# Performance work log

Hardware: AMD Instinct MI355X
Metric: run time of the kernel (lower is better)

Reference implementation:

```python
import jax, jax.numpy as jnp
import numpy as np

N, E = 50000, 600000
DIMS = [128, 256, 256, 256, 256, 64]  # in, h1..h4, out


def setup_inputs() -> dict:
    key = jax.random.key(0)
    ks = jax.random.split(key, 12)
    inp = {
        "x": jax.random.normal(ks[0], (N, DIMS[0]), dtype=jnp.float32),
        "edge_index": jax.random.randint(ks[1], (2, E), 0, N, dtype=jnp.int64 if jax.config.jax_enable_x64 else jnp.int32),
    }
    for i in range(5):
        fi, fo = DIMS[i], DIMS[i + 1]
        s = 1.0 / np.sqrt(fi)  # glorot-ish uniform, matching GCNConv default scale
        inp[f"W{i+1}"] = jax.random.uniform(ks[2 + 2 * i], (fi, fo), jnp.float32, -s, s)
        inp[f"b{i+1}"] = jnp.zeros((fo,), jnp.float32)
    return inp


def _gcn_norm(edge_index, n):
    # Add self-loops and compute symmetric normalization D^-1/2 (A+I) D^-1/2.
    loop = jnp.arange(n, dtype=edge_index.dtype)
    src = jnp.concatenate([edge_index[0], loop])  # [E+N]
    dst = jnp.concatenate([edge_index[1], loop])
    deg = jax.ops.segment_sum(jnp.ones_like(dst, dtype=jnp.float32), dst, num_segments=n)
    dinv = jnp.where(deg > 0, jax.lax.rsqrt(deg), 0.0)
    norm = dinv[src] * dinv[dst]  # [E+N]
    return src, dst, norm


def _gcn_layer(x, src, dst, norm, W, b, n):
    h = x @ W                       # [N, Fo] linear transform first (fewer msg bytes)
    msg = h[src] * norm[:, None]    # gather + edge-weight scale
    out = jax.ops.segment_sum(msg, dst, num_segments=n)  # scatter-add aggregate
    return out + b


def reference(x, edge_index, W1, b1, W2, b2, W3, b3, W4, b4, W5, b5):
    n = x.shape[0]
    src, dst, norm = _gcn_norm(edge_index, n)
    params = [(W1, b1), (W2, b2), (W3, b3), (W4, b4), (W5, b5)]
    h = x
    for i, (W, b) in enumerate(params):
        h = _gcn_layer(h, src, dst, norm, W, b, n)
        if i < 4:
            h = jax.nn.relu(h)  # dropout is identity in eval mode
    return h
```

## Files before the change

kernel.cpp:

```cpp
#include <hip/hip_runtime.h>
#include <stdint.h>


typedef _Float16 v8h __attribute__((ext_vector_type(8)));
typedef _Float16 v4h __attribute__((ext_vector_type(4)));
typedef float v4f __attribute__((ext_vector_type(4)));

__global__ void count_edges(const int* __restrict__ dst, int E, int* __restrict__ counts) {
    int i = blockIdx.x * blockDim.x + threadIdx.x;
    if (i < E) atomicAdd(&counts[dst[i]], 1);
}

__global__ void block_sums(const int* __restrict__ counts, int n, int* __restrict__ partial) {
    __shared__ int red[256];
    int t = threadIdx.x;
    int i = blockIdx.x * 256 + t;
    red[t] = (i < n) ? counts[i] : 0;
    __syncthreads();
    #pragma unroll
    for (int off = 128; off > 0; off >>= 1) {
        if (t < off) red[t] += red[t + off];
        __syncthreads();
    }
    if (t == 0) partial[blockIdx.x] = red[0];
}

__global__ void scan_partials(int* __restrict__ partial, int nb, int* __restrict__ row_ptr, int n) {
    __shared__ int s[256];
    int t = threadIdx.x;
    int v = (t < nb) ? partial[t] : 0;
    s[t] = v;
    __syncthreads();
    #pragma unroll
    for (int off = 1; off < 256; off <<= 1) {
        int u = (t >= off) ? s[t - off] : 0;
        __syncthreads();
        s[t] += u;
        __syncthreads();
    }
    if (t < nb) partial[t] = s[t] - v;
    if (t == 0) row_ptr[n] = s[255];
}

__global__ void scan_final(const int* __restrict__ counts, int n, const int* __restrict__ partial,
                           int* __restrict__ row_ptr, float* __restrict__ dinv,
                           int* __restrict__ fill) {
    __shared__ int s[256];
    int t = threadIdx.x;
    int i = blockIdx.x * 256 + t;
    int c = (i < n) ? counts[i] : 0;
    s[t] = c;
    __syncthreads();
    #pragma unroll
    for (int off = 1; off < 256; off <<= 1) {
        int u = (t >= off) ? s[t - off] : 0;
        __syncthreads();
        s[t] += u;
        __syncthreads();
    }
    if (i < n) {
        row_ptr[i] = partial[blockIdx.x] + s[t] - c;
        dinv[i] = rsqrtf((float)(c + 1));
        fill[i] = 0;
    }
}

__global__ void build_csr(const int* __restrict__ src, const int* __restrict__ dst, int E,
                          const int* __restrict__ row_ptr, int* __restrict__ fill,
                          int* __restrict__ ssrc) {
    int i = blockIdx.x * blockDim.x + threadIdx.x;
    if (i < E) {
        int d = dst[i];
        int pos = row_ptr[d] + atomicAdd(&fill[d], 1);
        ssrc[pos] = src[i];
    }
}

__global__ void split_w(const float* __restrict__ W, _Float16* __restrict__ Wh,
                        _Float16* __restrict__ Wl, int FI, int FO) {
    int i = blockIdx.x * 256 + threadIdx.x;
    if (i < FI * FO) {
        int c = i / FI, k = i - c * FI;
        float v = W[(size_t)k * FO + c];
        _Float16 h = (_Float16)v;
        Wh[i] = h;
        Wl[i] = (_Float16)(v - (float)h);
    }
}

template <int F, bool HILO_IN, bool SPLIT_OUT>
__global__ void agg_kernel(const float* __restrict__ inF,
                           const _Float16* __restrict__ inH, const _Float16* __restrict__ inL,
                           const int* __restrict__ row_ptr, const int* __restrict__ ssrc,
                           const float* __restrict__ dinv, const float* __restrict__ bias,
                           _Float16* __restrict__ outH, _Float16* __restrict__ outL,
                           float* __restrict__ outF, int n) {
    constexpr int VE = F / 64;
    int wid = (blockIdx.x * blockDim.x + threadIdx.x) >> 6;
    if (wid >= n) return;
    int lane = threadIdx.x & 63;
    const float dd = dinv[wid];
    float acc[VE];

    auto load_row = [&](int row, float* v) {
        if constexpr (HILO_IN) {
            v4h h = *(const v4h*)&inH[(size_t)row * F + lane * 4];
            v4h l = *(const v4h*)&inL[(size_t)row * F + lane * 4];
            #pragma unroll
            for (int j = 0; j < 4; ++j) v[j] = (float)h[j] + (float)l[j];
        } else if constexpr (VE == 4) {
            float4 t = *(const float4*)&inF[(size_t)row * F + lane * 4];
            v[0] = t.x; v[1] = t.y; v[2] = t.z; v[3] = t.w;
        } else if constexpr (VE == 2) {
            float2 t = *(const float2*)&inF[(size_t)row * F + lane * 2];
            v[0] = t.x; v[1] = t.y;
        } else {
            v[0] = inF[(size_t)row * F + lane];
        }
    };

    {
        float v[VE];
        load_row(wid, v);
        #pragma unroll
        for (int j = 0; j < VE; ++j) acc[j] = dd * v[j];
    }
    int e = row_ptr[wid];
    const int end = row_ptr[wid + 1];
    for (; e + 1 < end; e += 2) {
        int s0 = ssrc[e], s1 = ssrc[e + 1];
        float w0 = dinv[s0], w1 = dinv[s1];
        float v0[VE], v1[VE];
        load_row(s0, v0);
        load_row(s1, v1);
        #pragma unroll
        for (int j = 0; j < VE; ++j) acc[j] += w0 * v0[j];
        #pragma unroll
        for (int j = 0; j < VE; ++j) acc[j] += w1 * v1[j];
    }
    if (e < end) {
        int s = ssrc[e];
        float w = dinv[s];
        float v[VE];
        load_row(s, v);
        #pragma unroll
        for (int j = 0; j < VE; ++j) acc[j] += w * v[j];
    }

    if constexpr (SPLIT_OUT) {
        _Float16 hs[VE], ls[VE];
        #pragma unroll
        for (int j = 0; j < VE; ++j) {
            float s = dd * acc[j];
            _Float16 h = (_Float16)s;
            hs[j] = h;
            ls[j] = (_Float16)(s - (float)h);
        }
        size_t o = (size_t)wid * F + lane * VE;
        #pragma unroll
        for (int j = 0; j < VE; ++j) { outH[o + j] = hs[j]; outL[o + j] = ls[j]; }
    } else {
        #pragma unroll
        for (int j = 0; j < VE; ++j) {
            float s = dd * acc[j];
            if (bias) s += bias[lane * VE + j];
            outF[(size_t)wid * F + lane * VE + j] = s;
        }
    }
}

__device__ __forceinline__ void gl_lds16(const _Float16* g, _Float16* l) {
    __builtin_amdgcn_global_load_lds(
        (const __attribute__((address_space(1))) uint32_t*)g,
        (__attribute__((address_space(3))) uint32_t*)l, 16, 0, 0);
}

template <int FI, int FO, int MODE>
__global__ __launch_bounds__(256) void gemm_mfma(
    const _Float16* __restrict__ Ah, const _Float16* __restrict__ Al,
    const _Float16* __restrict__ Wth, const _Float16* __restrict__ Wtl,
    const float* __restrict__ bias,
    _Float16* __restrict__ Oh, _Float16* __restrict__ Ol,
    float* __restrict__ Of, int n) {
    constexpr int BK = 32;
    constexpr int NSTEP = FI / BK;
    __shared__ _Float16 lds[12288];
    const int m0 = blockIdx.x * 128;
    const int n0 = blockIdx.y * 64;
    const int t = threadIdx.x;
    const int w = t >> 6;
    const int lane = t & 63;

    const int G0 = w * 128 + lane;
    const int G1 = G0 + 64;
    const int arow0 = (G0 >> 6) * 16 + (G0 & 15), akc0 = ((G0 >> 4) & 3) * 8;
    const int arow1 = (G1 >> 6) * 16 + (G1 & 15), akc1 = ((G1 >> 4) & 3) * 8;
    const _Float16* sAh0 = Ah + (size_t)(m0 + arow0) * FI + akc0;
    const _Float16* sAh1 = Ah + (size_t)(m0 + arow1) * FI + akc1;
    const _Float16* sAl0 = Al + (size_t)(m0 + arow0) * FI + akc0;
    const _Float16* sAl1 = Al + (size_t)(m0 + arow1) * FI + akc1;
    const int bcol = w * 16 + (lane & 15), bkc = (lane >> 4) * 8;
    const _Float16* sBh = Wth + (size_t)(n0 + bcol) * FI + bkc;
    const _Float16* sBl = Wtl + (size_t)(n0 + bcol) * FI + bkc;

    _Float16* dAh0 = &lds[w * 1024];
    _Float16* dAh1 = &lds[w * 1024 + 512];
    _Float16* dAl0 = &lds[4096 + w * 1024];
    _Float16* dAl1 = &lds[4096 + w * 1024 + 512];
    _Float16* dBh = &lds[8192 + w * 512];
    _Float16* dBl = &lds[10240 + w * 512];

    const int wm = w >> 1, wn = w & 1;
    v4f acc[4][2];
    #pragma unroll
    for (int i = 0; i < 4; ++i)
        #pragma unroll
        for (int j = 0; j < 2; ++j) acc[i][j] = (v4f){0.f, 0.f, 0.f, 0.f};

    for (int s = 0; s < NSTEP; ++s) {
        const int ko = s * BK;
        gl_lds16(sAh0 + ko, dAh0);
        gl_lds16(sAh1 + ko, dAh1);
        gl_lds16(sAl0 + ko, dAl0);
        gl_lds16(sAl1 + ko, dAl1);
        gl_lds16(sBh + ko, dBh);
        gl_lds16(sBl + ko, dBl);
        __syncthreads();
        v8h ah[4], al[4], bh[2], bl[2];
        #pragma unroll
        for (int i = 0; i < 4; ++i) {
            ah[i] = *(const v8h*)&lds[(wm * 4 + i) * 512 + lane * 8];
            al[i] = *(const v8h*)&lds[4096 + (wm * 4 + i) * 512 + lane * 8];
        }
        #pragma unroll
        for (int j = 0; j < 2; ++j) {
            bh[j] = *(const v8h*)&lds[8192 + (wn * 2 + j) * 512 + lane * 8];
            bl[j] = *(const v8h*)&lds[10240 + (wn * 2 + j) * 512 + lane * 8];
        }
        #pragma unroll
        for (int i = 0; i < 4; ++i)
            #pragma unroll
            for (int j = 0; j < 2; ++j) {
                acc[i][j] = __builtin_amdgcn_mfma_f32_16x16x32_f16(ah[i], bh[j], acc[i][j], 0, 0, 0);
                acc[i][j] = __builtin_amdgcn_mfma_f32_16x16x32_f16(ah[i], bl[j], acc[i][j], 0, 0, 0);
                acc[i][j] = __builtin_amdgcn_mfma_f32_16x16x32_f16(al[i], bh[j], acc[i][j], 0, 0, 0);
            }
        __syncthreads();
    }

    const int rl = (lane >> 4) * 4;
    const int cl = lane & 15;
    #pragma unroll
    for (int j = 0; j < 2; ++j) {
        const int gcol = n0 + wn * 32 + j * 16 + cl;
        float bv = (MODE == 0) ? bias[gcol] : 0.f;
        #pragma unroll
        for (int i = 0; i < 4; ++i) {
            const int grow = m0 + wm * 64 + i * 16 + rl;
            #pragma unroll
            for (int r = 0; r < 4; ++r) {
                if (grow + r < n) {
                    float v = acc[i][j][r];
                    if (MODE == 0) {
                        v = fmaxf(v + bv, 0.f);
                        _Float16 h = (_Float16)v;
                        Oh[(size_t)(grow + r) * FO + gcol] = h;
                        Ol[(size_t)(grow + r) * FO + gcol] = (_Float16)(v - (float)h);
                    } else {
                        Of[(size_t)(grow + r) * FO + gcol] = v;
                    }
                }
            }
        }
    }
}

extern "C" void kernel_launch(void* const* d_in, const int* in_sizes, int n_in,
                              void* d_out, int out_size, void* d_ws, size_t ws_size,
                              hipStream_t stream) {
    const float* x = (const float*)d_in[0];
    const int* ei = (const int*)d_in[1];
    const int E = in_sizes[1] / 2;
    const int n = in_sizes[0] / 128;
    const int* esrc = ei;
    const int* edst = ei + E;
    const float* W[5] = {(const float*)d_in[2], (const float*)d_in[4], (const float*)d_in[6],
                         (const float*)d_in[8], (const float*)d_in[10]};
    const float* b[5] = {(const float*)d_in[3], (const float*)d_in[5], (const float*)d_in[7],
                         (const float*)d_in[9], (const float*)d_in[11]};
    float* out = (float*)d_out;
    const int NPAD = ((n + 127) / 128) * 128;

    char* ws = (char*)d_ws;
    auto carve = [&](size_t bytes) {
        char* p = ws;
        ws += (bytes + 255) & ~(size_t)255;
        return p;
    };
    int* counts = (int*)carve((size_t)n * 4);
    int* row_ptr = (int*)carve((size_t)(n + 1) * 4);
    int* fill = (int*)carve((size_t)n * 4);
    float* dinv = (float*)carve((size_t)n * 4);
    int* partial = (int*)carve(1024);
    int* ssrc = (int*)carve((size_t)E * 4);
    const int FIs[5] = {128, 256, 256, 256, 256};
    const int FOs[5] = {256, 256, 256, 256, 64};
    _Float16 *Wh[5], *Wl[5];
    for (int l = 0; l < 5; ++l) {
        Wh[l] = (_Float16*)carve((size_t)FIs[l] * FOs[l] * 2);
        Wl[l] = (_Float16*)carve((size_t)FIs[l] * FOs[l] * 2);
    }
    _Float16* Ah = (_Float16*)carve((size_t)NPAD * 256 * 2);
    _Float16* Al = (_Float16*)carve((size_t)NPAD * 256 * 2);
    _Float16* Bh = (_Float16*)carve((size_t)NPAD * 256 * 2);
    _Float16* Bl = (_Float16*)carve((size_t)NPAD * 256 * 2);
    float* scratch = (float*)Ah;

    hipMemsetAsync(counts, 0, (size_t)n * 4, stream);
    count_edges<<<(E + 255) / 256, 256, 0, stream>>>(edst, E, counts);
    const int nsb = (n + 255) / 256;
    block_sums<<<nsb, 256, 0, stream>>>(counts, n, partial);
    scan_partials<<<1, 256, 0, stream>>>(partial, nsb, row_ptr, n);
    scan_final<<<nsb, 256, 0, stream>>>(counts, n, partial, row_ptr, dinv, fill);
    build_csr<<<(E + 255) / 256, 256, 0, stream>>>(esrc, edst, E, row_ptr, fill, ssrc);
    for (int l = 0; l < 5; ++l) {
        int sz = FIs[l] * FOs[l];
        split_w<<<(sz + 255) / 256, 256, 0, stream>>>(W[l], Wh[l], Wl[l], FIs[l], FOs[l]);
    }

    const int aggBlocks = (n + 3) / 4;
    const dim3 g4(NPAD / 128, 4), g1(NPAD / 128, 1);

    agg_kernel<128, false, true><<<aggBlocks, 256, 0, stream>>>(
        x, nullptr, nullptr, row_ptr, ssrc, dinv, nullptr, Ah, Al, nullptr, n);
    gemm_mfma<128, 256, 0><<<g4, 256, 0, stream>>>(Ah, Al, Wh[0], Wl[0], b[0], Bh, Bl, nullptr, n);
    for (int l = 1; l < 4; ++l) {
        agg_kernel<256, true, true><<<aggBlocks, 256, 0, stream>>>(
            nullptr, Bh, Bl, row_ptr, ssrc, dinv, nullptr, Ah, Al, nullptr, n);
        gemm_mfma<256, 256, 0><<<g4, 256, 0, stream>>>(Ah, Al, Wh[l], Wl[l], b[l], Bh, Bl, nullptr, n);
    }
    gemm_mfma<256, 64, 1><<<g1, 256, 0, stream>>>(Bh, Bl, Wh[4], Wl[4], nullptr, nullptr, nullptr,
                                                  scratch, n);
    agg_kernel<64, false, false><<<aggBlocks, 256, 0, stream>>>(
        scratch, nullptr, nullptr, row_ptr, ssrc, dinv, b[4], nullptr, nullptr, out, n);
}
```

Measured before the change: 709.3 us.

## Pack hi/lo activations interleaved, precompute edge weights, widen GEMM tiles, fuse weight splits

The GEMM epilogue now writes hi/lo fp16 halves interleaved in one 32-bit word, so the aggregation kernel gathers each neighbour row with a single 16-byte load instead of two 8-byte loads. Per-edge normalisation weights are precomputed in CSR order, which removes the dependent dinv[src] gather in every aggregation. The 256-wide GEMM becomes one 64x256 tile per block so the A tile is loaded once rather than four times, the edge loop is unrolled by four, and the five weight-split launches are merged into one. The wider tile uses more LDS and accumulator registers, which may lower occupancy.

```diff
diff --git a/kernel.cpp b/kernel.cpp
--- a/kernel.cpp
+++ b/kernel.cpp
@@ -3,7 +3,6 @@
 
 
 typedef _Float16 v8h __attribute__((ext_vector_type(8)));
-typedef _Float16 v4h __attribute__((ext_vector_type(4)));
 typedef float v4f __attribute__((ext_vector_type(4)));
 
 __global__ void count_edges(const int* __restrict__ dst, int E, int* __restrict__ counts) {
@@ -67,34 +66,50 @@
 
 __global__ void build_csr(const int* __restrict__ src, const int* __restrict__ dst, int E,
                           const int* __restrict__ row_ptr, int* __restrict__ fill,
-                          int* __restrict__ ssrc) {
+                          int* __restrict__ ssrc, float* __restrict__ wsrc,
+                          const float* __restrict__ dinv) {
     int i = blockIdx.x * blockDim.x + threadIdx.x;
     if (i < E) {
         int d = dst[i];
+        int s = src[i];
         int pos = row_ptr[d] + atomicAdd(&fill[d], 1);
-        ssrc[pos] = src[i];
-    }
-}
-
-__global__ void split_w(const float* __restrict__ W, _Float16* __restrict__ Wh,
-                        _Float16* __restrict__ Wl, int FI, int FO) {
+        ssrc[pos] = s;
+        wsrc[pos] = dinv[s];
+    }
+}
+
+struct SplitArgs {
+    const float* W[5];
+    _Float16* Wh[5];
+    _Float16* Wl[5];
+    int lgFI[5];
+    int FO[5];
+    int off[6];
+};
+
+__global__ void split_all(SplitArgs a) {
     int i = blockIdx.x * 256 + threadIdx.x;
-    if (i < FI * FO) {
-        int c = i / FI, k = i - c * FI;
-        float v = W[(size_t)k * FO + c];
-        _Float16 h = (_Float16)v;
-        Wh[i] = h;
-        Wl[i] = (_Float16)(v - (float)h);
-    }
-}
-
-template <int F, bool HILO_IN, bool SPLIT_OUT>
-__global__ void agg_kernel(const float* __restrict__ inF,
-                           const _Float16* __restrict__ inH, const _Float16* __restrict__ inL,
-                           const int* __restrict__ row_ptr, const int* __restrict__ ssrc,
-                           const float* __restrict__ dinv, const float* __restrict__ bias,
-                           _Float16* __restrict__ outH, _Float16* __restrict__ outL,
-                           float* __restrict__ outF, int n) {
+    #pragma unroll
+    for (int l = 0; l < 5; ++l) {
+        if (i >= a.off[l] && i < a.off[l + 1]) {
+            int j = i - a.off[l];
+            int FI = 1 << a.lgFI[l];
+            int c = j >> a.lgFI[l];
+            int k = j & (FI - 1);
+            float v = a.W[l][(size_t)k * a.FO[l] + c];
+            _Float16 h = (_Float16)v;
+            a.Wh[l][j] = h;
+            a.Wl[l][j] = (_Float16)(v - (float)h);
+        }
+    }
+}
+
+template <int F, bool SPLIT_OUT>
+__global__ void agg_f32(const float* __restrict__ in, const int* __restrict__ row_ptr,
+                        const int* __restrict__ ssrc, const float* __restrict__ wsrc,
+                        const float* __restrict__ dinv, const float* __restrict__ bias,
+                        _Float16* __restrict__ outH, _Float16* __restrict__ outL,
+                        float* __restrict__ outF, int n) {
     constexpr int VE = F / 64;
     int wid = (blockIdx.x * blockDim.x + threadIdx.x) >> 6;
     if (wid >= n) return;
@@ -102,70 +117,112 @@
     const float dd = dinv[wid];
     float acc[VE];
 
-    auto load_row = [&](int row, float* v) {
-        if constexpr (HILO_IN) {
-            v4h h = *(const v4h*)&inH[(size_t)row * F + lane * 4];
-            v4h l = *(const v4h*)&inL[(size_t)row * F + lane * 4];
-            #pragma unroll
-            for (int j = 0; j < 4; ++j) v[j] = (float)h[j] + (float)l[j];
-        } else if constexpr (VE == 4) {
-            float4 t = *(const float4*)&inF[(size_t)row * F + lane * 4];
-            v[0] = t.x; v[1] = t.y; v[2] = t.z; v[3] = t.w;
-        } else if constexpr (VE == 2) {
-            float2 t = *(const float2*)&inF[(size_t)row * F + lane * 2];
+    auto loadrow = [&](int row, float* v) {
+        if constexpr (VE == 2) {
+            float2 t = *(const float2*)&in[(size_t)row * F + lane * 2];
             v[0] = t.x; v[1] = t.y;
         } else {
-            v[0] = inF[(size_t)row * F + lane];
+            v[0] = in[(size_t)row * F + lane];
         }
     };
 
     {
         float v[VE];
-        load_row(wid, v);
+        loadrow(wid, v);
         #pragma unroll
         for (int j = 0; j < VE; ++j) acc[j] = dd * v[j];
     }
     int e = row_ptr[wid];
     const int end = row_ptr[wid + 1];
-    for (; e + 1 < end; e += 2) {
-        int s0 = ssrc[e], s1 = ssrc[e + 1];
-        float w0 = dinv[s0], w1 = dinv[s1];
-        float v0[VE], v1[VE];
-        load_row(s0, v0);
-        load_row(s1, v1);
-        #pragma unroll
-        for (int j = 0; j < VE; ++j) acc[j] += w0 * v0[j];
-        #pragma unroll
-        for (int j = 0; j < VE; ++j) acc[j] += w1 * v1[j];
-    }
-    if (e < end) {
+    for (; e + 4 <= end; e += 4) {
+        int s0 = ssrc[e], s1 = ssrc[e + 1], s2 = ssrc[e + 2], s3 = ssrc[e + 3];
+        float w0 = wsrc[e], w1 = wsrc[e + 1], w2 = wsrc[e + 2], w3 = wsrc[e + 3];
+        float v0[VE], v1[VE], v2[VE], v3[VE];
+        loadrow(s0, v0); loadrow(s1, v1); loadrow(s2, v2); loadrow(s3, v3);
+        #pragma unroll
+        for (int j = 0; j < VE; ++j) acc[j] += w0 * v0[j] + w1 * v1[j];
+        #pragma unroll
+        for (int j = 0; j < VE; ++j) acc[j] += w2 * v2[j] + w3 * v3[j];
+    }
+    for (; e < end; ++e) {
         int s = ssrc[e];
-        float w = dinv[s];
+        float w = wsrc[e];
         float v[VE];
-        load_row(s, v);
+        loadrow(s, v);
         #pragma unroll
         for (int j = 0; j < VE; ++j) acc[j] += w * v[j];
     }
 
     if constexpr (SPLIT_OUT) {
-        _Float16 hs[VE], ls[VE];
+        size_t o = (size_t)wid * F + lane * VE;
         #pragma unroll
         for (int j = 0; j < VE; ++j) {
             float s = dd * acc[j];
             _Float16 h = (_Float16)s;
-            hs[j] = h;
-            ls[j] = (_Float16)(s - (float)h);
-        }
-        size_t o = (size_t)wid * F + lane * VE;
-        #pragma unroll
-        for (int j = 0; j < VE; ++j) { outH[o + j] = hs[j]; outL[o + j] = ls[j]; }
+            outH[o + j] = h;
+            outL[o + j] = (_Float16)(s - (float)h);
+        }
     } else {
         #pragma unroll
         for (int j = 0; j < VE; ++j) {
-            float s = dd * acc[j];
-            if (bias) s += bias[lane * VE + j];
+            float s = dd * acc[j] + bias[lane * VE + j];
             outF[(size_t)wid * F + lane * VE + j] = s;
         }
+    }
+}
+
+__global__ void agg_packed(const _Float16* __restrict__ inP, const int* __restrict__ row_ptr,
+                           const int* __restrict__ ssrc, const float* __restrict__ wsrc,
+                           const float* __restrict__ dinv,
+                           _Float16* __restrict__ outH, _Float16* __restrict__ outL, int n) {
+    int wid = (blockIdx.x * blockDim.x + threadIdx.x) >> 6;
+    if (wid >= n) return;
+    int lane = threadIdx.x & 63;
+    const float dd = dinv[wid];
+    float acc[4];
+
+    auto loadrow = [&](int row, float* v) {
+        v8h p = *(const v8h*)&inP[(size_t)row * 512 + lane * 8];
+        v[0] = (float)p[0] + (float)p[1];
+        v[1] = (float)p[2] + (float)p[3];
+        v[2] = (float)p[4] + (float)p[5];
+        v[3] = (float)p[6] + (float)p[7];
+    };
+
+    {
+        float v[4];
+        loadrow(wid, v);
+        #pragma unroll
+        for (int j = 0; j < 4; ++j) acc[j] = dd * v[j];
+    }
+    int e = row_ptr[wid];
+    const int end = row_ptr[wid + 1];
+    for (; e + 4 <= end; e += 4) {
+        int s0 = ssrc[e], s1 = ssrc[e + 1], s2 = ssrc[e + 2], s3 = ssrc[e + 3];
+        float w0 = wsrc[e], w1 = wsrc[e + 1], w2 = wsrc[e + 2], w3 = wsrc[e + 3];
+        float v0[4], v1[4], v2[4], v3[4];
+        loadrow(s0, v0); loadrow(s1, v1); loadrow(s2, v2); loadrow(s3, v3);
+        #pragma unroll
+        for (int j = 0; j < 4; ++j) acc[j] += w0 * v0[j] + w1 * v1[j];
+        #pragma unroll
+        for (int j = 0; j < 4; ++j) acc[j] += w2 * v2[j] + w3 * v3[j];
+    }
+    for (; e < end; ++e) {
+        int s = ssrc[e];
+        float w = wsrc[e];
+        float v[4];
+        loadrow(s, v);
+        #pragma unroll
+        for (int j = 0; j < 4; ++j) acc[j] += w * v[j];
+    }
+
+    size_t o = (size_t)wid * 256 + lane * 4;
+    #pragma unroll
+    for (int j = 0; j < 4; ++j) {
+        float s = dd * acc[j];
+        _Float16 h = (_Float16)s;
+        outH[o + j] = h;
+        outL[o + j] = (_Float16)(s - (float)h);
     }
 }
 
@@ -175,18 +232,114 @@
         (__attribute__((address_space(3))) uint32_t*)l, 16, 0, 0);
 }
 
-template <int FI, int FO, int MODE>
-__global__ __launch_bounds__(256) void gemm_mfma(
+template <int FI, int OUTMODE>
+__global__ __launch_bounds__(256) void gemm_wide(
     const _Float16* __restrict__ Ah, const _Float16* __restrict__ Al,
     const _Float16* __restrict__ Wth, const _Float16* __restrict__ Wtl,
     const float* __restrict__ bias,
-    _Float16* __restrict__ Oh, _Float16* __restrict__ Ol,
-    float* __restrict__ Of, int n) {
+    uint32_t* __restrict__ Opk, _Float16* __restrict__ Oh, _Float16* __restrict__ Ol,
+    int n) {
     constexpr int BK = 32;
     constexpr int NSTEP = FI / BK;
+    __shared__ _Float16 lds[20480];
+    const int m0 = blockIdx.x * 64;
+    const int t = threadIdx.x;
+    const int w = t >> 6;
+    const int lane = t & 63;
+
+    const int G = w * 64 + lane;
+    const int arow = (G >> 6) * 16 + (G & 15), akc = ((G >> 4) & 3) * 8;
+    const _Float16* sAh = Ah + (size_t)(m0 + arow) * FI + akc;
+    const _Float16* sAl = Al + (size_t)(m0 + arow) * FI + akc;
+    _Float16* dAh = &lds[w * 512];
+    _Float16* dAl = &lds[2048 + w * 512];
+    const int bq = lane & 15, bk = (lane >> 4) * 8;
+    const _Float16* sB[4];
+    _Float16* dBh[4];
+    _Float16* dBl[4];
+    #pragma unroll
+    for (int q = 0; q < 4; ++q) {
+        int sub = w * 4 + q;
+        sB[q] = (const _Float16*)((size_t)(sub * 16 + bq) * FI + bk);
+        dBh[q] = &lds[4096 + sub * 512];
+        dBl[q] = &lds[12288 + sub * 512];
+    }
+
+    v4f acc[4][4];
+    #pragma unroll
+    for (int i = 0; i < 4; ++i)
+        #pragma unroll
+        for (int j = 0; j < 4; ++j) acc[i][j] = (v4f){0.f, 0.f, 0.f, 0.f};
+
+    for (int s = 0; s < NSTEP; ++s) {
+        const int ko = s * BK;
+        gl_lds16(sAh + ko, dAh);
+        gl_lds16(sAl + ko, dAl);
+        #pragma unroll
+        for (int q = 0; q < 4; ++q) {
+            size_t off = (size_t)sB[q];
+            gl_lds16(Wth + off + ko, dBh[q]);
+            gl_lds16(Wtl + off + ko, dBl[q]);
+        }
+        __syncthreads();
+        v8h ahf[4], alf[4], bhf[4], blf[4];
+        #pragma unroll
+        for (int i = 0; i < 4; ++i) {
+            ahf[i] = *(const v8h*)&lds[i * 512 + lane * 8];
+            alf[i] = *(const v8h*)&lds[2048 + i * 512 + lane * 8];
+        }
+        #pragma unroll
+        for (int j = 0; j < 4; ++j) {
+            bhf[j] = *(const v8h*)&lds[4096 + (w * 4 + j) * 512 + lane * 8];
+            blf[j] = *(const v8h*)&lds[12288 + (w * 4 + j) * 512 + lane * 8];
+        }
+        #pragma unroll
+        for (int i = 0; i < 4; ++i)
+            #pragma unroll
+            for (int j = 0; j < 4; ++j) {
+                acc[i][j] = __builtin_amdgcn_mfma_f32_16x16x32_f16(ahf[i], bhf[j], acc[i][j], 0, 0, 0);
+                acc[i][j] = __builtin_amdgcn_mfma_f32_16x16x32_f16(ahf[i], blf[j], acc[i][j], 0, 0, 0);
+                acc[i][j] = __builtin_amdgcn_mfma_f32_16x16x32_f16(alf[i], bhf[j], acc[i][j], 0, 0, 0);
+            }
+        __syncthreads();
+    }
+
+    const int rl = (lane >> 4) * 4;
+    const int cl = lane & 15;
+    #pragma unroll
+    for (int j = 0; j < 4; ++j) {
+        const int gcol = w * 64 + j * 16 + cl;
+        const float bv = bias[gcol];
+        #pragma unroll
+        for (int i = 0; i < 4; ++i) {
+            const int grow = m0 + i * 16 + rl;
+            #pragma unroll
+            for (int r = 0; r < 4; ++r) {
+                if (grow + r < n) {
+                    float v = fmaxf(acc[i][j][r] + bv, 0.f);
+                    _Float16 h = (_Float16)v;
+                    _Float16 l = (_Float16)(v - (float)h);
+                    if (OUTMODE == 0) {
+                        uint32_t u = (uint32_t)__builtin_bit_cast(uint16_t, h) |
+                                     ((uint32_t)__builtin_bit_cast(uint16_t, l) << 16);
+                        Opk[(size_t)(grow + r) * 256 + gcol] = u;
+                    } else {
+                        Oh[(size_t)(grow + r) * 256 + gcol] = h;
+                        Ol[(size_t)(grow + r) * 256 + gcol] = l;
+                    }
+                }
+            }
+        }
+    }
+}
+
+__global__ __launch_bounds__(256) void gemm_narrow(
+    const _Float16* __restrict__ Ah, const _Float16* __restrict__ Al,
+    const _Float16* __restrict__ Wth, const _Float16* __restrict__ Wtl,
+    float* __restrict__ Of, int n) {
+    constexpr int FI = 256, FO = 64;
     __shared__ _Float16 lds[12288];
     const int m0 = blockIdx.x * 128;
-    const int n0 = blockIdx.y * 64;
     const int t = threadIdx.x;
     const int w = t >> 6;
     const int lane = t & 63;
@@ -200,8 +353,8 @@
     const _Float16* sAl0 = Al + (size_t)(m0 + arow0) * FI + akc0;
     const _Float16* sAl1 = Al + (size_t)(m0 + arow1) * FI + akc1;
     const int bcol = w * 16 + (lane & 15), bkc = (lane >> 4) * 8;
-    const _Float16* sBh = Wth + (size_t)(n0 + bcol) * FI + bkc;
-    const _Float16* sBl = Wtl + (size_t)(n0 + bcol) * FI + bkc;
+    const _Float16* sBh = Wth + (size_t)bcol * FI + bkc;
+    const _Float16* sBl = Wtl + (size_t)bcol * FI + bkc;
 
     _Float16* dAh0 = &lds[w * 1024];
     _Float16* dAh1 = &lds[w * 1024 + 512];
@@ -217,8 +370,8 @@
         #pragma unroll
         for (int j = 0; j < 2; ++j) acc[i][j] = (v4f){0.f, 0.f, 0.f, 0.f};
 
-    for (int s = 0; s < NSTEP; ++s) {
-        const int ko = s * BK;
+    for (int s = 0; s < 8; ++s) {
+        const int ko = s * 32;
         gl_lds16(sAh0 + ko, dAh0);
         gl_lds16(sAh1 + ko, dAh1);
         gl_lds16(sAl0 + ko, dAl0);
@@ -252,25 +405,13 @@
     const int cl = lane & 15;
     #pragma unroll
     for (int j = 0; j < 2; ++j) {
-        const int gcol = n0 + wn * 32 + j * 16 + cl;
-        float bv = (MODE == 0) ? bias[gcol] : 0.f;
+        const int gcol = wn * 32 + j * 16 + cl;
         #pragma unroll
         for (int i = 0; i < 4; ++i) {
             const int grow = m0 + wm * 64 + i * 16 + rl;
             #pragma unroll
-            for (int r = 0; r < 4; ++r) {
-                if (grow + r < n) {
-                    float v = acc[i][j][r];
-                    if (MODE == 0) {
-                        v = fmaxf(v + bv, 0.f);
-                        _Float16 h = (_Float16)v;
-                        Oh[(size_t)(grow + r) * FO + gcol] = h;
-                        Ol[(size_t)(grow + r) * FO + gcol] = (_Float16)(v - (float)h);
-                    } else {
-                        Of[(size_t)(grow + r) * FO + gcol] = v;
-                    }
-                }
-            }
+            for (int r = 0; r < 4; ++r)
+                if (grow + r < n) Of[(size_t)(grow + r) * FO + gcol] = acc[i][j][r];
         }
     }
 }
@@ -284,8 +425,6 @@
     const int n = in_sizes[0] / 128;
     const int* esrc = ei;
     const int* edst = ei + E;
-    const float* W[5] = {(const float*)d_in[2], (const float*)d_in[4], (const float*)d_in[6],
-                         (const float*)d_in[8], (const float*)d_in[10]};
     const float* b[5] = {(const float*)d_in[3], (const float*)d_in[5], (const float*)d_in[7],
                          (const float*)d_in[9], (const float*)d_in[11]};
     float* out = (float*)d_out;
@@ -303,6 +442,7 @@
     float* dinv = (float*)carve((size_t)n * 4);
     int* partial = (int*)carve(1024);
     int* ssrc = (int*)carve((size_t)E * 4);
+    float* wsrc = (float*)carve((size_t)E * 4);
     const int FIs[5] = {128, 256, 256, 256, 256};
     const int FOs[5] = {256, 256, 256, 256, 64};
     _Float16 *Wh[5], *Wl[5];
@@ -312,8 +452,9 @@
     }
     _Float16* Ah = (_Float16*)carve((size_t)NPAD * 256 * 2);
     _Float16* Al = (_Float16*)carve((size_t)NPAD * 256 * 2);
-    _Float16* Bh = (_Float16*)carve((size_t)NPAD * 256 * 2);
-    _Float16* Bl = (_Float16*)carve((size_t)NPAD * 256 * 2);
+    uint32_t* Ppk = (uint32_t*)carve((size_t)NPAD * 256 * 4);
+    _Float16* Bh2 = (_Float16*)Ppk;
+    _Float16* Bl2 = (_Float16*)Ppk + (size_t)NPAD * 256;
     float* scratch = (float*)Ah;
 
     hipMemsetAsync(counts, 0, (size_t)n * 4, stream);
@@ -322,25 +463,38 @@
     block_sums<<<nsb, 256, 0, stream>>>(counts, n, partial);
     scan_partials<<<1, 256, 0, stream>>>(partial, nsb, row_ptr, n);
     scan_final<<<nsb, 256, 0, stream>>>(counts, n, partial, row_ptr, dinv, fill);
-    build_csr<<<(E + 255) / 256, 256, 0, stream>>>(esrc, edst, E, row_ptr, fill, ssrc);
+    build_csr<<<(E + 255) / 256, 256, 0, stream>>>(esrc, edst, E, row_ptr, fill, ssrc, wsrc, dinv);
+
+    SplitArgs sa;
+    int off = 0;
     for (int l = 0; l < 5; ++l) {
-        int sz = FIs[l] * FOs[l];
-        split_w<<<(sz + 255) / 256, 256, 0, stream>>>(W[l], Wh[l], Wl[l], FIs[l], FOs[l]);
-    }
+        sa.W[l] = (const float*)d_in[2 + 2 * l];
+        sa.Wh[l] = Wh[l];
+        sa.Wl[l] = Wl[l];
+        sa.lgFI[l] = (FIs[l] == 128) ? 7 : 8;
+        sa.FO[l] = FOs[l];
+        sa.off[l] = off;
+        off += FIs[l] * FOs[l];
+    }
+    sa.off[5] = off;
+    split_all<<<(off + 255) / 256, 256, 0, stream>>>(sa);
 
     const int aggBlocks = (n + 3) / 4;
-    const dim3 g4(NPAD / 128, 4), g1(NPAD / 128, 1);
-
-    agg_kernel<128, false, true><<<aggBlocks, 256, 0, stream>>>(
-        x, nullptr, nullptr, row_ptr, ssrc, dinv, nullptr, Ah, Al, nullptr, n);
-    gemm_mfma<128, 256, 0><<<g4, 256, 0, stream>>>(Ah, Al, Wh[0], Wl[0], b[0], Bh, Bl, nullptr, n);
-    for (int l = 1; l < 4; ++l) {
-        agg_kernel<256, true, true><<<aggBlocks, 256, 0, stream>>>(
-            nullptr, Bh, Bl, row_ptr, ssrc, dinv, nullptr, Ah, Al, nullptr, n);
-        gemm_mfma<256, 256, 0><<<g4, 256, 0, stream>>>(Ah, Al, Wh[l], Wl[l], b[l], Bh, Bl, nullptr, n);
-    }
-    gemm_mfma<256, 64, 1><<<g1, 256, 0, stream>>>(Bh, Bl, Wh[4], Wl[4], nullptr, nullptr, nullptr,
-                                                  scratch, n);
-    agg_kernel<64, false, false><<<aggBlocks, 256, 0, stream>>>(
-        scratch, nullptr, nullptr, row_ptr, ssrc, dinv, b[4], nullptr, nullptr, out, n);
-}
+    const int gw = NPAD / 64;
+    const int gn = NPAD / 128;
+
+    agg_f32<128, true><<<aggBlocks, 256, 0, stream>>>(x, row_ptr, ssrc, wsrc, dinv, nullptr,
+                                                      Ah, Al, nullptr, n);
+    gemm_wide<128, 0><<<gw, 256, 0, stream>>>(Ah, Al, Wh[0], Wl[0], b[0], Ppk, nullptr, nullptr, n);
+    for (int l = 1; l <= 2; ++l) {
+        agg_packed<<<aggBlocks, 256, 0, stream>>>((const _Float16*)Ppk, row_ptr, ssrc, wsrc, dinv,
+                                                  Ah, Al, n);
+        gemm_wide<256, 0><<<gw, 256, 0, stream>>>(Ah, Al, Wh[l], Wl[l], b[l], Ppk, nullptr, nullptr, n);
+    }
+    agg_packed<<<aggBlocks, 256, 0, stream>>>((const _Float16*)Ppk, row_ptr, ssrc, wsrc, dinv,
+                                              Ah, Al, n);
+    gemm_wide<256, 1><<<gw, 256, 0, stream>>>(Ah, Al, Wh[3], Wl[3], b[3], nullptr, Bh2, Bl2, n);
+    gemm_narrow<<<gn, 256, 0, stream>>>(Bh2, Bl2, Wh[4], Wl[4], scratch, n);
+    agg_f32<64, false><<<aggBlocks, 256, 0, stream>>>(scratch, row_ptr, ssrc, wsrc, dinv, b[4],
+                                                      nullptr, nullptr, out, n);
+}
```

Result: faster. 692.7 us (-2.3%).
